# Performance work log

Hardware: AMD Instinct MI355X
Metric: run time of the kernel (lower is better)

## Reference

```python
import jax, jax.numpy as jnp
import numpy as np

L, B, T, D, H = 4, 16, 512, 512, 8
DK = D // H
DF = 2048


def layer_norm(x, w, b, eps=1e-5):
    mu = jnp.mean(x, axis=-1, keepdims=True)
    var = jnp.mean(jnp.square(x - mu), axis=-1, keepdims=True)
    return (x - mu) * jax.lax.rsqrt(var + eps) * w + b


def rel_shift(x):
    # legacy Transformer-XL shift; x: (B, H, T1, T2)
    b, h, t1, t2 = x.shape
    zp = jnp.zeros((b, h, t1, 1), x.dtype)
    xp = jnp.concatenate([zp, x], axis=-1).reshape(b, h, t2 + 1, t1)
    return xp[:, :, 1:, :].reshape(b, h, t1, t2)


def setup_inputs() -> dict:
    key = jax.random.key(0)
    ks = jax.random.split(key, 16)
    s = 1.0 / np.sqrt(D)
    sf = 1.0 / np.sqrt(DF)
    return {
        "mask": jnp.ones((B, 1, T), dtype=bool),
        "xs": jax.random.normal(ks[0], (B, T, D), jnp.float32),
        "pos_emb": jax.random.normal(ks[1], (1, T, D), jnp.float32),
        "ln_mha_w": jnp.ones((L, D), jnp.float32),
        "ln_mha_b": jnp.zeros((L, D), jnp.float32),
        "wq": jax.random.normal(ks[2], (L, D, D), jnp.float32) * s,
        "bq": jnp.zeros((L, D), jnp.float32),
        "wk": jax.random.normal(ks[3], (L, D, D), jnp.float32) * s,
        "bk": jnp.zeros((L, D), jnp.float32),
        "wv": jax.random.normal(ks[4], (L, D, D), jnp.float32) * s,
        "bv": jnp.zeros((L, D), jnp.float32),
        "wp": jax.random.normal(ks[5], (L, D, D), jnp.float32) * s,
        "pos_bias_u": jax.random.normal(ks[6], (L, H, DK), jnp.float32) * 0.02,
        "pos_bias_v": jax.random.normal(ks[7], (L, H, DK), jnp.float32) * 0.02,
        "wo": jax.random.normal(ks[8], (L, D, D), jnp.float32) * s,
        "bo": jnp.zeros((L, D), jnp.float32),
        "ln_ff_w": jnp.ones((L, D), jnp.float32),
        "ln_ff_b": jnp.zeros((L, D), jnp.float32),
        "w1": jax.random.normal(ks[9], (L, DF, D), jnp.float32) * s,
        "b1": jnp.zeros((L, DF), jnp.float32),
        "w2": jax.random.normal(ks[10], (L, D, DF), jnp.float32) * sf,
        "b2": jnp.zeros((L, D), jnp.float32),
        "after_norm_w": jnp.ones((D,), jnp.float32),
        "after_norm_b": jnp.zeros((D,), jnp.float32),
    }


def reference(mask, xs, pos_emb, ln_mha_w, ln_mha_b, wq, bq, wk, bk, wv, bv,
              wp, pos_bias_u, pos_bias_v, wo, bo, ln_ff_w, ln_ff_b,
              w1, b1, w2, b2, after_norm_w, after_norm_b):
    x = xs
    m = mask[:, None, :, :]  # (B,1,1,T) broadcast over heads and query dim
    neg = jnp.finfo(x.dtype).min
    scale = 1.0 / np.sqrt(DK)
    for i in range(L):
        # --- relative-position multi-head self-attention (pre-norm) ---
        xn = layer_norm(x, ln_mha_w[i], ln_mha_b[i])
        q = (xn @ wq[i].T + bq[i]).reshape(B, T, H, DK)
        k = (xn @ wk[i].T + bk[i]).reshape(B, T, H, DK)
        v = (xn @ wv[i].T + bv[i]).reshape(B, T, H, DK)
        p = (pos_emb @ wp[i].T).reshape(1, T, H, DK)
        q_u = q + pos_bias_u[i]  # (B,T,H,DK)
        q_v = q + pos_bias_v[i]
        matrix_ac = jnp.einsum("bthd,bshd->bhts", q_u, k)
        matrix_bd = jnp.einsum("bthd,nshd->bhts", q_v, p)
        matrix_bd = rel_shift(matrix_bd)
        scores = (matrix_ac + matrix_bd) * scale  # (B,H,T,T)
        scores = jnp.where(m, scores, neg)
        attn = jax.nn.softmax(scores, axis=-1)
        attn = jnp.where(m, attn, 0.0)
        ctx = jnp.einsum("bhts,bshd->bthd", attn, v).reshape(B, T, D)
        x = x + ctx @ wo[i].T + bo[i]
        # --- feed-forward (pre-norm) ---
        xn = layer_norm(x, ln_ff_w[i], ln_ff_b[i])
        h = jax.nn.relu(xn @ w1[i].T + b1[i])
        x = x + h @ w2[i].T + b2[i]
    return layer_norm(x, after_norm_w, after_norm_b)
```

## Files before the change

kernel.cpp:

```cpp
#include <hip/hip_runtime.h>

typedef long long i64;
typedef unsigned short u16;
typedef __attribute__((ext_vector_type(8))) short bf16x8;
typedef __attribute__((ext_vector_type(8))) unsigned short u16x8;
typedef __attribute__((ext_vector_type(4))) unsigned short u16x4;
typedef __attribute__((ext_vector_type(4))) float f32x4;

#define L_  4
#define B_  16
#define T_  512
#define D_  512
#define H_  8
#define DK_ 64
#define DF_ 2048
#define QKSTR 1024

#define WLSTRIDE 3407872

__device__ __forceinline__ u16 f2b(float f) {
    unsigned u = __float_as_uint(f);
    u += 0x7FFF + ((u >> 16) & 1);
    return (u16)(u >> 16);
}
__device__ __forceinline__ float b2f(u16 b) {
    return __uint_as_float(((unsigned)b) << 16);
}
__device__ __forceinline__ void gld16(const void* g, void* l) {
    __builtin_amdgcn_global_load_lds(
        (const __attribute__((address_space(1))) void*)g,
        (__attribute__((address_space(3))) void*)l, 16, 0, 0);
}

__global__ __launch_bounds__(256) void cvt1_k(const float* __restrict__ s,
                                              u16* __restrict__ d, int n4)
{
    int id = blockIdx.x * 256 + threadIdx.x;
    if (id >= n4) return;
    float4 u = reinterpret_cast<const float4*>(s)[id];
    u16x4 o; o[0] = f2b(u.x); o[1] = f2b(u.y); o[2] = f2b(u.z); o[3] = f2b(u.w);
    *reinterpret_cast<u16x4*>(d + (i64)id * 4) = o;
}

__global__ __launch_bounds__(256) void cvt7_k(
    const float* __restrict__ wq, const float* __restrict__ wk,
    const float* __restrict__ wv, const float* __restrict__ wp,
    const float* __restrict__ wo, const float* __restrict__ w1,
    const float* __restrict__ w2, u16* __restrict__ dst)
{
    int l = blockIdx.y;
    wq += (i64)l * 262144; wk += (i64)l * 262144; wv += (i64)l * 262144;
    wp += (i64)l * 262144; wo += (i64)l * 262144;
    w1 += (i64)l * 1048576; w2 += (i64)l * 1048576;
    dst += (i64)l * WLSTRIDE;
    int id = blockIdx.x * 256 + threadIdx.x;
    if (id >= 851968) return;
    const float* s; i64 doff;
    if (id < 327680) {
        int seg = id >> 16, off = id & 65535;
        s = seg == 0 ? wq : seg == 1 ? wk : seg == 2 ? wv : seg == 3 ? wp : wo;
        s += (i64)off * 4;
        doff = (i64)seg * 262144 + (i64)off * 4;
    } else {
        int id2 = id - 327680;
        int seg = id2 >> 18, off = id2 & 262143;
        s = (seg ? w2 : w1) + (i64)off * 4;
        doff = 1310720 + (i64)seg * 1048576 + (i64)off * 4;
    }
    float4 u = *reinterpret_cast<const float4*>(s);
    u16x4 o; o[0] = f2b(u.x); o[1] = f2b(u.y); o[2] = f2b(u.z); o[3] = f2b(u.w);
    *reinterpret_cast<u16x4*>(dst + doff) = o;
}

__global__ __launch_bounds__(256) void packb_k(const float* __restrict__ bq,
                                               const float* __restrict__ bk,
                                               const float* __restrict__ bv,
                                               float* __restrict__ dst)
{
    int id = blockIdx.x * 256 + threadIdx.x;
    if (id >= L_ * 1536) return;
    int l = id / 1536, c = id % 1536;
    float v = (c < 512) ? bq[l * 512 + c]
            : (c < 1024) ? bk[l * 512 + c - 512]
                         : bv[l * 512 + c - 1024];
    dst[id] = v;
}

template<bool OB>
__global__ __launch_bounds__(256) void ln_k(const float* __restrict__ x,
                                            const float* __restrict__ w,
                                            const float* __restrict__ b,
                                            void* __restrict__ outv, int nrows)
{
    int wid  = (blockIdx.x * 256 + threadIdx.x) >> 6;
    int lane = threadIdx.x & 63;
    if (wid >= nrows) return;
    const float* xr = x + (i64)wid * D_;
    float4 u = reinterpret_cast<const float4*>(xr)[lane * 2 + 0];
    float4 v = reinterpret_cast<const float4*>(xr)[lane * 2 + 1];
    float s = u.x + u.y + u.z + u.w + v.x + v.y + v.z + v.w;
    float q = u.x*u.x + u.y*u.y + u.z*u.z + u.w*u.w
            + v.x*v.x + v.y*v.y + v.z*v.z + v.w*v.w;
#pragma unroll
    for (int m = 1; m < 64; m <<= 1) { s += __shfl_xor(s, m); q += __shfl_xor(q, m); }
    float mu   = s * (1.0f / D_);
    float var  = q * (1.0f / D_) - mu * mu;
    float rstd = rsqrtf(var + 1e-5f);
    int c0 = lane * 8;
    float o[8];
    o[0] = (u.x - mu) * rstd * w[c0+0] + b[c0+0];
    o[1] = (u.y - mu) * rstd * w[c0+1] + b[c0+1];
    o[2] = (u.z - mu) * rstd * w[c0+2] + b[c0+2];
    o[3] = (u.w - mu) * rstd * w[c0+3] + b[c0+3];
    o[4] = (v.x - mu) * rstd * w[c0+4] + b[c0+4];
    o[5] = (v.y - mu) * rstd * w[c0+5] + b[c0+5];
    o[6] = (v.z - mu) * rstd * w[c0+6] + b[c0+6];
    o[7] = (v.w - mu) * rstd * w[c0+7] + b[c0+7];
    if (OB) {
        u16x8 ob;
#pragma unroll
        for (int i = 0; i < 8; i++) ob[i] = f2b(o[i]);
        *reinterpret_cast<u16x8*>((u16*)outv + (i64)wid * D_ + c0) = ob;
    } else {
        float4 o0 = {o[0], o[1], o[2], o[3]};
        float4 o1 = {o[4], o[5], o[6], o[7]};
        reinterpret_cast<float4*>((float*)outv + (i64)wid * D_)[lane * 2 + 0] = o0;
        reinterpret_cast<float4*>((float*)outv + (i64)wid * D_)[lane * 2 + 1] = o1;
    }
}

__global__ __launch_bounds__(256) void colbias_k(const u16* __restrict__ kb, int ld,
                                                 const float* __restrict__ pbias,
                                                 float* __restrict__ out, int ntok)
{
    int wid  = (blockIdx.x * 256 + threadIdx.x) >> 6;
    int l    = threadIdx.x & 63;
    if (wid >= ntok) return;
    int h = l >> 3, d0 = (l & 7) * 8;
    u16x8 kv = *reinterpret_cast<const u16x8*>(kb + (i64)wid * ld + h * 64 + d0);
    float s = 0.f;
#pragma unroll
    for (int i = 0; i < 8; i++) s += b2f(kv[i]) * pbias[h * 64 + d0 + i];
    s += __shfl_xor(s, 1); s += __shfl_xor(s, 2); s += __shfl_xor(s, 4);
    if ((l & 7) == 0) out[(i64)(wid >> 9) * 4096 + h * 512 + (wid & 511)] = s;
}

__global__ __launch_bounds__(256, 4) void fattn_k(
    const u16* __restrict__ qkv, const u16* __restrict__ vT_b,
    const float* __restrict__ acb, const u16* __restrict__ bds,
    u16* __restrict__ ctx)
{
    __shared__ u16 kbuf[2][64 * 64];
    __shared__ u16 vbuf[2][64 * 64];
    __shared__ u16 pbuf[64 * 64];

    const int id = blockIdx.x;
    const int h = id & 7, b = (id >> 3) & 15, qt = id >> 7;
    const int i0 = qt * 64;
    const int tid = threadIdx.x;
    const int w = tid >> 6, lane = tid & 63;
    const int lr = lane & 15, g = lane >> 4;
    const int lc = (lane & 7) ^ ((lane >> 3) & 7);

    bf16x8 qw[2];
#pragma unroll
    for (int kk = 0; kk < 2; ++kk)
        qw[kk] = *reinterpret_cast<const bf16x8*>(
            qkv + ((i64)b * T_ + i0 + w * 16 + lr) * QKSTR + h * DK_ + kk * 32 + g * 8);

    {
        const u16* ksrc = qkv + 512 + ((i64)b * T_) * QKSTR + h * DK_;
        const u16* vsrc = vT_b + ((i64)(b * H_ + h) * DK_) * T_;
#pragma unroll
        for (int t2 = 0; t2 < 2; ++t2) {
            int t = w * 2 + t2;
            gld16(ksrc + (i64)(t * 8 + (lane >> 3)) * QKSTR + lc * 8,
                  (char*)&kbuf[0][0] + t * 1024);
            gld16(vsrc + (i64)(t * 8 + (lane >> 3)) * T_ + lc * 8,
                  (char*)&vbuf[0][0] + t * 1024);
        }
    }
    __syncthreads();

    float mrun[4], lrun[4];
    f32x4 O[4];
#pragma unroll
    for (int qq = 0; qq < 4; ++qq) { mrun[qq] = -1e30f; lrun[qq] = 0.f; }
#pragma unroll
    for (int ni = 0; ni < 4; ++ni) O[ni] = {0.f, 0.f, 0.f, 0.f};

    const float* acbh = acb + (i64)b * (H_ * T_) + h * T_;
    const u16* bdsp = bds + (((i64)(b * H_ + h)) << 18)
                          + (i64)(i0 + w * 16 + g * 4) * T_;

    for (int jt = 0; jt < 8; ++jt) {
        if (jt) __syncthreads();
        const int cur = jt & 1;
        if (jt < 7) {
            int j0n = (jt + 1) * 64;
            const u16* ksrc = qkv + 512 + ((i64)b * T_ + j0n) * QKSTR + h * DK_;
            const u16* vsrc = vT_b + ((i64)(b * H_ + h) * DK_) * T_ + j0n;
#pragma unroll
            for (int t2 = 0; t2 < 2; ++t2) {
                int t = w * 2 + t2;
                gld16(ksrc + (i64)(t * 8 + (lane >> 3)) * QKSTR + lc * 8,
                      (char*)&kbuf[cur ^ 1][0] + t * 1024);
                gld16(vsrc + (i64)(t * 8 + (lane >> 3)) * T_ + lc * 8,
                      (char*)&vbuf[cur ^ 1][0] + t * 1024);
            }
        }
        const int j0 = jt * 64;

        u16 bdr[4][4];
        float acf[4];
#pragma unroll
        for (int ni = 0; ni < 4; ++ni) {
            acf[ni] = acbh[j0 + ni * 16 + lr];
#pragma unroll
            for (int qq = 0; qq < 4; ++qq)
                bdr[ni][qq] = bdsp[(i64)qq * T_ + j0 + ni * 16 + lr];
        }

        f32x4 S[4];
        __builtin_amdgcn_s_setprio(1);
#pragma unroll
        for (int ni = 0; ni < 4; ++ni) {
            int r = ni * 16 + lr;
            bf16x8 kf0 = *reinterpret_cast<const bf16x8*>(
                &kbuf[cur][0] + r * 64 + ((g ^ (r & 7)) * 8));
            bf16x8 kf1 = *reinterpret_cast<const bf16x8*>(
                &kbuf[cur][0] + r * 64 + (((4 + g) ^ (r & 7)) * 8));
            f32x4 acc = {0.f, 0.f, 0.f, 0.f};
            acc = __builtin_amdgcn_mfma_f32_16x16x32_bf16(qw[0], kf0, acc, 0, 0, 0);
            acc = __builtin_amdgcn_mfma_f32_16x16x32_bf16(qw[1], kf1, acc, 0, 0, 0);
            S[ni] = acc;
        }
        __builtin_amdgcn_s_setprio(0);
#pragma unroll
        for (int ni = 0; ni < 4; ++ni) {
            int j = j0 + ni * 16 + lr;
#pragma unroll
            for (int qq = 0; qq < 4; ++qq) {
                int rel = j - (i0 + w * 16 + g * 4 + qq);
                float bdv = (rel == 1) ? 0.f : b2f(bdr[ni][qq]);
                S[ni][qq] = (S[ni][qq] + acf[ni] + bdv) * 0.125f;
            }
        }
        float pmax[4];
#pragma unroll
        for (int qq = 0; qq < 4; ++qq) {
            float v0 = fmaxf(fmaxf(S[0][qq], S[1][qq]), fmaxf(S[2][qq], S[3][qq]));
            v0 = fmaxf(v0, __shfl_xor(v0, 1));
            v0 = fmaxf(v0, __shfl_xor(v0, 2));
            v0 = fmaxf(v0, __shfl_xor(v0, 4));
            v0 = fmaxf(v0, __shfl_xor(v0, 8));
            pmax[qq] = v0;
        }
        bool grow = (pmax[0] > mrun[0] + 8.f) | (pmax[1] > mrun[1] + 8.f)
                  | (pmax[2] > mrun[2] + 8.f) | (pmax[3] > mrun[3] + 8.f);
        if (__any(grow)) {
#pragma unroll
            for (int qq = 0; qq < 4; ++qq) {
                float mnew = fmaxf(mrun[qq], pmax[qq]);
                float alpha = __expf(mrun[qq] - mnew);
                mrun[qq] = mnew;
#pragma unroll
                for (int ni = 0; ni < 4; ++ni) O[ni][qq] *= alpha;
                lrun[qq] *= alpha;
            }
        }
#pragma unroll
        for (int qq = 0; qq < 4; ++qq) {
            float ls = 0.f;
#pragma unroll
            for (int ni = 0; ni < 4; ++ni) {
                float pv = __expf(S[ni][qq] - mrun[qq]);
                S[ni][qq] = pv;
                ls += pv;
            }
            ls += __shfl_xor(ls, 1); ls += __shfl_xor(ls, 2);
            ls += __shfl_xor(ls, 4); ls += __shfl_xor(ls, 8);
            lrun[qq] += ls;
        }
#pragma unroll
        for (int ni = 0; ni < 4; ++ni) {
#pragma unroll
            for (int qq = 0; qq < 4; ++qq) {
                int rp = w * 16 + g * 4 + qq;
                int col = ni * 16 + lr;
                pbuf[rp * 64 + (((col >> 3) ^ (rp & 7)) * 8) + (col & 7)] =
                    f2b(S[ni][qq]);
            }
        }
        __builtin_amdgcn_s_waitcnt(0xC07F);
        __builtin_amdgcn_s_setprio(1);
#pragma unroll
        for (int kk = 0; kk < 2; ++kk) {
            int r = w * 16 + lr;
            bf16x8 aP = *reinterpret_cast<const bf16x8*>(
                &pbuf[0] + r * 64 + (((kk * 4 + g) ^ (r & 7)) * 8));
#pragma unroll
            for (int ni = 0; ni < 4; ++ni) {
                int rv = ni * 16 + lr;
                bf16x8 vf = *reinterpret_cast<const bf16x8*>(
                    &vbuf[cur][0] + rv * 64 + (((kk * 4 + g) ^ (rv & 7)) * 8));
                O[ni] = __builtin_amdgcn_mfma_f32_16x16x32_bf16(aP, vf, O[ni], 0, 0, 0);
            }
        }
        __builtin_amdgcn_s_setprio(0);
    }

#pragma unroll
    for (int qq = 0; qq < 4; ++qq) {
        float inv = 1.0f / lrun[qq];
        int t = i0 + w * 16 + g * 4 + qq;
        u16* orow = ctx + ((i64)b * T_ + t) * D_ + h * DK_;
#pragma unroll
        for (int ni = 0; ni < 4; ++ni)
            orow[ni * 16 + lr] = f2b(O[ni][qq] * inv);
    }
}

template<int BN, bool QKVF, bool OUTB, bool BIAS, bool RELU, bool ADD, bool BDST>
__global__ __launch_bounds__(256) void gemm_k(
    const u16* __restrict__ Ag, int lda, i64 sAo, i64 sAi,
    const u16* __restrict__ Bg, int ldb, i64 sBo, i64 sBi,
    void* __restrict__ Cg, int ldc, i64 sCo, i64 sCi,
    const float* __restrict__ biasg, i64 sBiaso, i64 sBiasi,
    const float* __restrict__ adds,
    u16* __restrict__ vTg, float* __restrict__ acbg,
    const float* __restrict__ pbug,
    int innerB, int K)
{
    constexpr int BM   = 128;
    constexpr int WN   = BN / 2;
    constexpr int NFN  = WN / 16;
    constexpr int NISS = (BM + BN) / 64;
    __shared__ u16 sh[2][(BM + BN) * 32];

    int z  = blockIdx.z;
    int ob = z / innerB, ib = z % innerB;
    const u16*   A16 = Ag + ob * sAo + ib * sAi;
    const u16*   Bp  = Bg + ob * sBo + ib * sBi;
    float*       Cf  = (float*)Cg + ob * sCo + ib * sCi;
    u16*         Cb  = (u16*)Cg + ob * sCo + ib * sCi;
    const float* bias = BIAS ? (biasg + ob * sBiaso + ib * sBiasi) : nullptr;
    const float* Asrc = ADD ? (adds + ob * sCo + ib * sCi) : nullptr;

    int tid = threadIdx.x;
    int w = tid >> 6, l = tid & 63;
    int row0 = blockIdx.x * BM, col0 = blockIdx.y * BN;
    int wr = (w >> 1) * 64, wc = (w & 1) * WN;
    int lr = l & 15, g = l >> 4;
    int swz = (lr >> 1) & 3;

    int frb = w * 16 + (l >> 2);
    int cjk = l & 3;

    f32x4 acc[4][NFN];
#pragma unroll
    for (int mi = 0; mi < 4; ++mi)
#pragma unroll
        for (int ni = 0; ni < NFN; ++ni)
#pragma unroll
            for (int j = 0; j < 4; ++j) acc[mi][ni][j] = 0.f;

    const int nt = K / 32;

    auto STAGE = [&](int d, int kt) {
        int k0 = kt * 32;
#pragma unroll
        for (int t = 0; t < NISS; ++t) {
            int R = t * 64 + frb;
            int ccs = (cjk ^ ((R >> 1) & 3)) * 8;
            const u16* src = (R < BM) ? (A16 + (i64)(row0 + R) * lda + k0 + ccs)
                                      : (Bp  + (i64)(col0 + R - BM) * ldb + k0 + ccs);
            gld16(src, (char*)&sh[d][0] + t * 4096 + w * 1024);
        }
    };

    STAGE(0, 0);
    for (int t = 0; t < nt; ++t) {
        const int cur = t & 1;
        __syncthreads();
        if (t + 1 < nt) STAGE(cur ^ 1, t + 1);
        bf16x8 av[4], bv[NFN];
#pragma unroll
        for (int mi = 0; mi < 4; ++mi) {
            int r = wr + mi * 16 + lr;
            av[mi] = *reinterpret_cast<const bf16x8*>(
                (char*)&sh[cur][0] + r * 64 + ((g ^ swz) * 16));
        }
#pragma unroll
        for (int ni = 0; ni < NFN; ++ni) {
            int r = wc + ni * 16 + lr;
            bv[ni] = *reinterpret_cast<const bf16x8*>(
                (char*)&sh[cur][0] + BM * 64 + r * 64 + ((g ^ swz) * 16));
        }
#pragma unroll
        for (int mi = 0; mi < 4; ++mi)
#pragma unroll
            for (int ni = 0; ni < NFN; ++ni)
                acc[mi][ni] = __builtin_amdgcn_mfma_f32_16x16x32_bf16(
                    av[mi], bv[ni], acc[mi][ni], 0, 0, 0);
    }

    if constexpr (QKVF) {
        __shared__ float redbuf[2][64];
        if (col0 >= 1024) {
            int h = (col0 - 1024) >> 6;
#pragma unroll
            for (int mi = 0; mi < 4; ++mi) {
                int r0 = row0 + wr + mi * 16 + g * 4;
                int bb = r0 >> 9, t0 = r0 & 511;
#pragma unroll
                for (int ni = 0; ni < NFN; ++ni) {
                    int d = wc + ni * 16 + lr;
                    u16x4 o;
#pragma unroll
                    for (int q = 0; q < 4; ++q)
                        o[q] = f2b(acc[mi][ni][q] + bias[col0 + d]);
                    *reinterpret_cast<u16x4*>(
                        vTg + ((i64)(bb * 8 + h) * 64 + d) * T_ + t0) = o;
                }
            }
            __syncthreads();
        } else {
            const bool kreg = col0 >= 512;
            int h = (col0 - 512) >> 6;
            float psum[4][4];
#pragma unroll
            for (int mi = 0; mi < 4; ++mi)
#pragma unroll
                for (int q = 0; q < 4; ++q) psum[mi][q] = 0.f;
#pragma unroll
            for (int mi = 0; mi < 4; ++mi) {
#pragma unroll
                for (int ni = 0; ni < NFN; ++ni) {
                    int c = col0 + wc + ni * 16 + lr;
                    float pb = kreg ? pbug[h * 64 + wc + ni * 16 + lr] : 0.f;
#pragma unroll
                    for (int q = 0; q < 4; ++q) {
                        int r = row0 + wr + mi * 16 + g * 4 + q;
                        float vv = acc[mi][ni][q] + bias[c];
                        Cb[(i64)r * QKSTR + c] = f2b(vv);
                        psum[mi][q] += vv * pb;
                    }
                }
            }
            if (kreg) {
#pragma unroll
                for (int mi = 0; mi < 4; ++mi)
#pragma unroll
                    for (int q = 0; q < 4; ++q) {
                        psum[mi][q] += __shfl_xor(psum[mi][q], 1);
                        psum[mi][q] += __shfl_xor(psum[mi][q], 2);
                        psum[mi][q] += __shfl_xor(psum[mi][q], 4);
                        psum[mi][q] += __shfl_xor(psum[mi][q], 8);
                    }
                if ((w & 1) == 1 && lr == 0) {
#pragma unroll
                    for (int mi = 0; mi < 4; ++mi)
#pragma unroll
                        for (int q = 0; q < 4; ++q)
                            redbuf[w >> 1][mi * 16 + g * 4 + q] = psum[mi][q];
                }
            }
            __syncthreads();
            if (kreg && (w & 1) == 0 && lr == 0) {
#pragma unroll
                for (int mi = 0; mi < 4; ++mi)
#pragma unroll
                    for (int q = 0; q < 4; ++q) {
                        int lrow = mi * 16 + g * 4 + q;
                        int r = row0 + wr + lrow;
                        float tot = psum[mi][q] + redbuf[w >> 1][lrow];
                        acbg[(i64)(r >> 9) * 4096 + h * 512 + (r & 511)] = tot;
                    }
            }
        }
    } else {
#pragma unroll
        for (int mi = 0; mi < 4; ++mi) {
#pragma unroll
            for (int ni = 0; ni < NFN; ++ni) {
#pragma unroll
                for (int q = 0; q < 4; ++q) {
                    int r = row0 + wr + mi * 16 + g * 4 + q;
                    int c = col0 + wc + ni * 16 + lr;
                    float vv = acc[mi][ni][q];
                    if (BIAS) vv += bias[c];
                    if (BDST) {
                        if (c >= T_ - 1 - r)
                            Cb[(i64)r * T_ + (c - (T_ - 1) + r)] = f2b(vv);
                        else if (r >= 1)
                            Cb[(i64)(r - 1) * T_ + (c + r + 1)] = f2b(vv);
                    } else {
                        if (ADD)  vv += Asrc[(i64)r * ldc + c];
                        if (RELU) vv = vv > 0.f ? vv : 0.f;
                        if (OUTB) Cb[(i64)r * ldc + c] = f2b(vv);
                        else      Cf[(i64)r * ldc + c] = vv;
                    }
                }
            }
        }
    }
}

extern "C" void kernel_launch(void* const* d_in, const int* in_sizes, int n_in,
                              void* d_out, int out_size, void* d_ws, size_t ws_size,
                              hipStream_t stream)
{
    const float* xs        = (const float*)d_in[1];
    const float* pos_emb   = (const float*)d_in[2];
    const float* ln_mha_w  = (const float*)d_in[3];
    const float* ln_mha_b  = (const float*)d_in[4];
    const float* wq        = (const float*)d_in[5];
    const float* bq        = (const float*)d_in[6];
    const float* wk        = (const float*)d_in[7];
    const float* bk        = (const float*)d_in[8];
    const float* wv        = (const float*)d_in[9];
    const float* bv        = (const float*)d_in[10];
    const float* wp        = (const float*)d_in[11];
    const float* pbu       = (const float*)d_in[12];
    const float* pbv       = (const float*)d_in[13];
    const float* wo        = (const float*)d_in[14];
    const float* bo        = (const float*)d_in[15];
    const float* ln_ff_w   = (const float*)d_in[16];
    const float* ln_ff_b   = (const float*)d_in[17];
    const float* w1        = (const float*)d_in[18];
    const float* b1        = (const float*)d_in[19];
    const float* w2        = (const float*)d_in[20];
    const float* b2        = (const float*)d_in[21];
    const float* anw       = (const float*)d_in[22];
    const float* anb       = (const float*)d_in[23];

    const i64 NTOK = (i64)B_ * T_;
    const i64 XSZ  = NTOK * D_;

    float* ws = (float*)d_ws;
    i64 off = 0;
    float* x    = ws + off;            off += XSZ;
    u16*  h_b   = (u16*)(ws + off);    off += NTOK * DF_ / 2;
    u16*  bds   = (u16*)(ws + off);    off += (i64)B_*H_*T_*T_/2;
    u16*  qk    = (u16*)(ws + off);    off += NTOK * QKSTR / 2;
    u16*  xn_b  = (u16*)(ws + off);    off += XSZ / 2;
    u16*  vT_b  = (u16*)(ws + off);    off += XSZ / 2;
    u16*  p_all = (u16*)(ws + off);    off += (i64)L_*T_*D_ / 2;
    u16*  pos_b = (u16*)(ws + off);    off += (i64)T_*D_ / 2;
    u16*  wl_b  = (u16*)(ws + off);    off += (i64)L_ * WLSTRIDE / 2;
    float* acb  = ws + off;            off += (i64)B_*H_*T_;
    float* bdb  = ws + off;            off += (i64)L_*H_*T_;
    float* bqkv = ws + off;            off += (i64)L_*1536;

    dim3 blk(256);
    dim3 gLN(2048);
    dim3 gQKV(64, 24, 1);
    dim3 gN64(64, 8, 1);
    dim3 gP(4, 4, 4);
    dim3 gBD(4, 4, 128);
    dim3 gFA(1024, 1, 1);
    dim3 gFF1(64, 16, 1);

    const i64 sBT = (i64)T_ * QKSTR;

    cvt1_k<<<256, blk, 0, stream>>>(pos_emb, pos_b, 65536);
    cvt7_k<<<dim3(3328, 4), blk, 0, stream>>>(wq, wk, wv, wp, wo, w1, w2, wl_b);
    packb_k<<<24, blk, 0, stream>>>(bq, bk, bv, bqkv);

    gemm_k<128,false,true,false,false,false,false><<<gP, blk, 0, stream>>>(
        pos_b, D_, 0, 0, wl_b + 786432, D_, WLSTRIDE, 0,
        p_all, D_, (i64)T_*D_, 0, nullptr, 0, 0,
        nullptr, nullptr, nullptr, nullptr, 1, D_);
    for (int l = 0; l < L_; l++)
        colbias_k<<<128, blk, 0, stream>>>(
            p_all + (i64)l*T_*D_, D_, pbv + (i64)l*H_*DK_, bdb + (i64)l*H_*T_, T_);

    for (int l = 0; l < L_; l++) {
        u16* wl = wl_b + (i64)l * WLSTRIDE;
        const float* xin = (l == 0) ? xs : x;

        ln_k<true><<<gLN, blk, 0, stream>>>(xin, ln_mha_w + l*D_, ln_mha_b + l*D_, xn_b, (int)NTOK);

        gemm_k<64,true,false,true,false,false,false><<<gQKV, blk, 0, stream>>>(
            xn_b, D_, 0, 0, wl + 0, D_, 0, 0, qk, QKSTR, 0, 0,
            bqkv + l*1536, 0, 0, nullptr, vT_b, acb, pbu + (i64)l*H_*DK_, 1, D_);

        gemm_k<128,false,false,true,false,false,true><<<gBD, blk, 0, stream>>>(
            qk, QKSTR, sBT, DK_, p_all + (i64)l*T_*D_, D_, 0, DK_,
            bds, T_, (i64)H_ * T_ * T_, (i64)T_ * T_,
            bdb + (i64)l*H_*T_, 0, T_, nullptr, nullptr, nullptr, nullptr, H_, DK_);

        fattn_k<<<gFA, blk, 0, stream>>>(qk, vT_b, acb, bds, xn_b);

        gemm_k<64,false,false,true,false,true,false><<<gN64, blk, 0, stream>>>(
            xn_b, D_, 0, 0, wl + 1048576, D_, 0, 0, x, D_, 0, 0,
            bo + l*D_, 0, 0, xin, nullptr, nullptr, nullptr, 1, D_);

        ln_k<true><<<gLN, blk, 0, stream>>>(x, ln_ff_w + l*D_, ln_ff_b + l*D_, xn_b, (int)NTOK);

        gemm_k<128,false,true,true,true,false,false><<<gFF1, blk, 0, stream>>>(
            xn_b, D_, 0, 0, wl + 1310720, D_, 0, 0, h_b, DF_, 0, 0,
            b1 + l*DF_, 0, 0, nullptr, nullptr, nullptr, nullptr, 1, D_);
        gemm_k<64,false,false,true,false,true,false><<<gN64, blk, 0, stream>>>(
            h_b, DF_, 0, 0, wl + 2359296, DF_, 0, 0, x, D_, 0, 0,
            b2 + l*D_, 0, 0, x, nullptr, nullptr, nullptr, 1, DF_);
    }

    ln_k<false><<<gLN, blk, 0, stream>>>(x, anw, anb, d_out, (int)NTOK);
}
```

Before: 727.9 us.

## Fold ac-bias and exp2 scale into BD store; add BK=64 GEMM tiles

The per-column ac bias and the softmax scale times log2(e) are now folded into the BD GEMM epilogue. The attention kernel therefore does one FMA per score and uses exp2f, and it no longer loads the ac bias in every tile. The rel==1 diagonal term is precomputed per row. The GEMM kernel gains a BK template parameter, and the two N=64 residual GEMMs use BK=64 to halve the K-loop iterations and barriers. The cost is double the shared memory for those GEMMs, plus a larger lazy-rescale threshold that has to keep fp32 from overflowing.

```diff
diff --git a/kernel.cpp b/kernel.cpp
--- a/kernel.cpp
+++ b/kernel.cpp
@@ -17,6 +17,7 @@
 #define QKSTR 1024
 
 #define WLSTRIDE 3407872
+#define SC2E 0.1803368801111f
 
 __device__ __forceinline__ u16 f2b(float f) {
     unsigned u = __float_as_uint(f);
@@ -168,6 +169,14 @@
         qw[kk] = *reinterpret_cast<const bf16x8*>(
             qkv + ((i64)b * T_ + i0 + w * 16 + lr) * QKSTR + h * DK_ + kk * 32 + g * 8);
 
+    const float* acbh = acb + (i64)b * (H_ * T_) + h * T_;
+    float acd[4];
+#pragma unroll
+    for (int qq = 0; qq < 4; ++qq) {
+        int jd = i0 + w * 16 + g * 4 + qq + 1;
+        acd[qq] = (jd < 512) ? acbh[jd] * SC2E : 0.f;
+    }
+
     {
         const u16* ksrc = qkv + 512 + ((i64)b * T_) * QKSTR + h * DK_;
         const u16* vsrc = vT_b + ((i64)(b * H_ + h) * DK_) * T_;
@@ -189,7 +198,6 @@
 #pragma unroll
     for (int ni = 0; ni < 4; ++ni) O[ni] = {0.f, 0.f, 0.f, 0.f};
 
-    const float* acbh = acb + (i64)b * (H_ * T_) + h * T_;
     const u16* bdsp = bds + (((i64)(b * H_ + h)) << 18)
                           + (i64)(i0 + w * 16 + g * 4) * T_;
 
@@ -212,14 +220,11 @@
         const int j0 = jt * 64;
 
         u16 bdr[4][4];
-        float acf[4];
-#pragma unroll
-        for (int ni = 0; ni < 4; ++ni) {
-            acf[ni] = acbh[j0 + ni * 16 + lr];
+#pragma unroll
+        for (int ni = 0; ni < 4; ++ni)
 #pragma unroll
             for (int qq = 0; qq < 4; ++qq)
                 bdr[ni][qq] = bdsp[(i64)qq * T_ + j0 + ni * 16 + lr];
-        }
 
         f32x4 S[4];
         __builtin_amdgcn_s_setprio(1);
@@ -242,8 +247,8 @@
 #pragma unroll
             for (int qq = 0; qq < 4; ++qq) {
                 int rel = j - (i0 + w * 16 + g * 4 + qq);
-                float bdv = (rel == 1) ? 0.f : b2f(bdr[ni][qq]);
-                S[ni][qq] = (S[ni][qq] + acf[ni] + bdv) * 0.125f;
+                float bdv = (rel == 1) ? acd[qq] : b2f(bdr[ni][qq]);
+                S[ni][qq] = fmaf(S[ni][qq], SC2E, bdv);
             }
         }
         float pmax[4];
@@ -256,13 +261,13 @@
             v0 = fmaxf(v0, __shfl_xor(v0, 8));
             pmax[qq] = v0;
         }
-        bool grow = (pmax[0] > mrun[0] + 8.f) | (pmax[1] > mrun[1] + 8.f)
-                  | (pmax[2] > mrun[2] + 8.f) | (pmax[3] > mrun[3] + 8.f);
+        bool grow = (pmax[0] > mrun[0] + 11.5f) | (pmax[1] > mrun[1] + 11.5f)
+                  | (pmax[2] > mrun[2] + 11.5f) | (pmax[3] > mrun[3] + 11.5f);
         if (__any(grow)) {
 #pragma unroll
             for (int qq = 0; qq < 4; ++qq) {
                 float mnew = fmaxf(mrun[qq], pmax[qq]);
-                float alpha = __expf(mrun[qq] - mnew);
+                float alpha = exp2f(mrun[qq] - mnew);
                 mrun[qq] = mnew;
 #pragma unroll
                 for (int ni = 0; ni < 4; ++ni) O[ni][qq] *= alpha;
@@ -274,7 +279,7 @@
             float ls = 0.f;
 #pragma unroll
             for (int ni = 0; ni < 4; ++ni) {
-                float pv = __expf(S[ni][qq] - mrun[qq]);
+                float pv = exp2f(S[ni][qq] - mrun[qq]);
                 S[ni][qq] = pv;
                 ls += pv;
             }
@@ -321,7 +326,7 @@
     }
 }
 
-template<int BN, bool QKVF, bool OUTB, bool BIAS, bool RELU, bool ADD, bool BDST>
+template<int BN, int BK, bool QKVF, bool OUTB, bool BIAS, bool RELU, bool ADD, bool BDST>
 __global__ __launch_bounds__(256) void gemm_k(
     const u16* __restrict__ Ag, int lda, i64 sAo, i64 sAi,
     const u16* __restrict__ Bg, int ldb, i64 sBo, i64 sBi,
@@ -335,8 +340,11 @@
     constexpr int BM   = 128;
     constexpr int WN   = BN / 2;
     constexpr int NFN  = WN / 16;
-    constexpr int NISS = (BM + BN) / 64;
-    __shared__ u16 sh[2][(BM + BN) * 32];
+    constexpr int CH   = BK / 8;
+    constexpr int KK   = BK / 32;
+    constexpr int RS   = BK * 2;
+    constexpr int NISS = (BM + BN) * CH / 256;
+    __shared__ u16 sh[2][(BM + BN) * BK];
 
     int z  = blockIdx.z;
     int ob = z / innerB, ib = z % innerB;
@@ -352,10 +360,10 @@
     int row0 = blockIdx.x * BM, col0 = blockIdx.y * BN;
     int wr = (w >> 1) * 64, wc = (w & 1) * WN;
     int lr = l & 15, g = l >> 4;
-    int swz = (lr >> 1) & 3;
-
-    int frb = w * 16 + (l >> 2);
-    int cjk = l & 3;
+    int rk = (BK == 32) ? ((lr >> 1) & 3) : (lr & 7);
+
+    int frb = tid / CH;
+    int cjk = tid % CH;
 
     f32x4 acc[4][NFN];
 #pragma unroll
@@ -365,14 +373,15 @@
 #pragma unroll
             for (int j = 0; j < 4; ++j) acc[mi][ni][j] = 0.f;
 
-    const int nt = K / 32;
+    const int nt = K / BK;
 
     auto STAGE = [&](int d, int kt) {
-        int k0 = kt * 32;
+        int k0 = kt * BK;
 #pragma unroll
         for (int t = 0; t < NISS; ++t) {
-            int R = t * 64 + frb;
-            int ccs = (cjk ^ ((R >> 1) & 3)) * 8;
+            int R = t * (256 / CH) + frb;
+            int key = (BK == 32) ? ((R >> 1) & 3) : (R & 7);
+            int ccs = (cjk ^ key) * 8;
             const u16* src = (R < BM) ? (A16 + (i64)(row0 + R) * lda + k0 + ccs)
                                       : (Bp  + (i64)(col0 + R - BM) * ldb + k0 + ccs);
             gld16(src, (char*)&sh[d][0] + t * 4096 + w * 1024);
@@ -384,25 +393,31 @@
         const int cur = t & 1;
         __syncthreads();
         if (t + 1 < nt) STAGE(cur ^ 1, t + 1);
-        bf16x8 av[4], bv[NFN];
+        bf16x8 av[4][KK], bv[NFN][KK];
 #pragma unroll
         for (int mi = 0; mi < 4; ++mi) {
             int r = wr + mi * 16 + lr;
-            av[mi] = *reinterpret_cast<const bf16x8*>(
-                (char*)&sh[cur][0] + r * 64 + ((g ^ swz) * 16));
+#pragma unroll
+            for (int kk = 0; kk < KK; ++kk)
+                av[mi][kk] = *reinterpret_cast<const bf16x8*>(
+                    (char*)&sh[cur][0] + r * RS + (((kk * 4 + g) ^ rk) * 16));
         }
 #pragma unroll
         for (int ni = 0; ni < NFN; ++ni) {
             int r = wc + ni * 16 + lr;
-            bv[ni] = *reinterpret_cast<const bf16x8*>(
-                (char*)&sh[cur][0] + BM * 64 + r * 64 + ((g ^ swz) * 16));
-        }
-#pragma unroll
-        for (int mi = 0; mi < 4; ++mi)
-#pragma unroll
-            for (int ni = 0; ni < NFN; ++ni)
-                acc[mi][ni] = __builtin_amdgcn_mfma_f32_16x16x32_bf16(
-                    av[mi], bv[ni], acc[mi][ni], 0, 0, 0);
+#pragma unroll
+            for (int kk = 0; kk < KK; ++kk)
+                bv[ni][kk] = *reinterpret_cast<const bf16x8*>(
+                    (char*)&sh[cur][0] + BM * RS + r * RS + (((kk * 4 + g) ^ rk) * 16));
+        }
+#pragma unroll
+        for (int kk = 0; kk < KK; ++kk)
+#pragma unroll
+            for (int mi = 0; mi < 4; ++mi)
+#pragma unroll
+                for (int ni = 0; ni < NFN; ++ni)
+                    acc[mi][ni] = __builtin_amdgcn_mfma_f32_16x16x32_bf16(
+                        av[mi][kk], bv[ni][kk], acc[mi][ni], 0, 0, 0);
     }
 
     if constexpr (QKVF) {
@@ -480,6 +495,8 @@
             }
         }
     } else {
+        const float* acz = BDST ? ((const float*)acbg + (i64)ob * 4096 + ib * 512)
+                                : nullptr;
 #pragma unroll
         for (int mi = 0; mi < 4; ++mi) {
 #pragma unroll
@@ -491,10 +508,13 @@
                     float vv = acc[mi][ni][q];
                     if (BIAS) vv += bias[c];
                     if (BDST) {
-                        if (c >= T_ - 1 - r)
-                            Cb[(i64)r * T_ + (c - (T_ - 1) + r)] = f2b(vv);
-                        else if (r >= 1)
-                            Cb[(i64)(r - 1) * T_ + (c + r + 1)] = f2b(vv);
+                        if (c >= T_ - 1 - r) {
+                            int j = c - (T_ - 1) + r;
+                            Cb[(i64)r * T_ + j] = f2b((vv + acz[j]) * SC2E);
+                        } else if (r >= 1) {
+                            int j = c + r + 1;
+                            Cb[(i64)(r - 1) * T_ + j] = f2b((vv + acz[j]) * SC2E);
+                        }
                     } else {
                         if (ADD)  vv += Asrc[(i64)r * ldc + c];
                         if (RELU) vv = vv > 0.f ? vv : 0.f;
@@ -568,7 +588,7 @@
     cvt7_k<<<dim3(3328, 4), blk, 0, stream>>>(wq, wk, wv, wp, wo, w1, w2, wl_b);
     packb_k<<<24, blk, 0, stream>>>(bq, bk, bv, bqkv);
 
-    gemm_k<128,false,true,false,false,false,false><<<gP, blk, 0, stream>>>(
+    gemm_k<128,32,false,true,false,false,false,false><<<gP, blk, 0, stream>>>(
         pos_b, D_, 0, 0, wl_b + 786432, D_, WLSTRIDE, 0,
         p_all, D_, (i64)T_*D_, 0, nullptr, 0, 0,
         nullptr, nullptr, nullptr, nullptr, 1, D_);
@@ -582,27 +602,27 @@
 
         ln_k<true><<<gLN, blk, 0, stream>>>(xin, ln_mha_w + l*D_, ln_mha_b + l*D_, xn_b, (int)NTOK);
 
-        gemm_k<64,true,false,true,false,false,false><<<gQKV, blk, 0, stream>>>(
+        gemm_k<64,32,true,false,true,false,false,false><<<gQKV, blk, 0, stream>>>(
             xn_b, D_, 0, 0, wl + 0, D_, 0, 0, qk, QKSTR, 0, 0,
             bqkv + l*1536, 0, 0, nullptr, vT_b, acb, pbu + (i64)l*H_*DK_, 1, D_);
 
-        gemm_k<128,false,false,true,false,false,true><<<gBD, blk, 0, stream>>>(
+        gemm_k<128,32,false,false,true,false,false,true><<<gBD, blk, 0, stream>>>(
             qk, QKSTR, sBT, DK_, p_all + (i64)l*T_*D_, D_, 0, DK_,
             bds, T_, (i64)H_ * T_ * T_, (i64)T_ * T_,
-            bdb + (i64)l*H_*T_, 0, T_, nullptr, nullptr, nullptr, nullptr, H_, DK_);
+            bdb + (i64)l*H_*T_, 0, T_, nullptr, nullptr, acb, nullptr, H_, DK_);
 
         fattn_k<<<gFA, blk, 0, stream>>>(qk, vT_b, acb, bds, xn_b);
 
-        gemm_k<64,false,false,true,false,true,false><<<gN64, blk, 0, stream>>>(
+        gemm_k<64,64,false,false,true,false,true,false><<<gN64, blk, 0, stream>>>(
             xn_b, D_, 0, 0, wl + 1048576, D_, 0, 0, x, D_, 0, 0,
             bo + l*D_, 0, 0, xin, nullptr, nullptr, nullptr, 1, D_);
 
         ln_k<true><<<gLN, blk, 0, stream>>>(x, ln_ff_w + l*D_, ln_ff_b + l*D_, xn_b, (int)NTOK);
 
-        gemm_k<128,false,true,true,true,false,false><<<gFF1, blk, 0, stream>>>(
+        gemm_k<128,32,false,true,true,true,false,false><<<gFF1, blk, 0, stream>>>(
             xn_b, D_, 0, 0, wl + 1310720, D_, 0, 0, h_b, DF_, 0, 0,
             b1 + l*DF_, 0, 0, nullptr, nullptr, nullptr, nullptr, 1, D_);
-        gemm_k<64,false,false,true,false,true,false><<<gN64, blk, 0, stream>>>(
+        gemm_k<64,64,false,false,true,false,true,false><<<gN64, blk, 0, stream>>>(
             h_b, DF_, 0, 0, wl + 2359296, DF_, 0, 0, x, D_, 0, 0,
             b2 + l*D_, 0, 0, x, nullptr, nullptr, nullptr, 1, DF_);
     }
```

New measurement: 823.5 us. +13.1%, slower.
